# Performance work log

Measured on AMD Instinct MI355X. Metric: run time of the kernel, lower is better.

The kernel has to match this reference:

```python
import jax, jax.numpy as jnp
import numpy as np

R = 16
LORA_ALPHA = 16
SCALING = LORA_ALPHA / R  # 1.0


def setup_inputs() -> dict:
    key = jax.random.key(0)
    kx, kr, ka = jax.random.split(key, 3)
    B, S, D, DO, E = 4, 2048, 4096, 4096, 8
    x = jax.random.normal(kx, (B, S, D), dtype=jnp.float32)
    # kaiming_uniform_(a=sqrt(5)) on Linear weight of fan_in=D -> U(-1/sqrt(D), 1/sqrt(D))
    bound_r = 1.0 / np.sqrt(D)
    route_w = jax.random.uniform(kr, (E, D), jnp.float32, -bound_r, bound_r)  # lora_route.weight
    bound_a = 1.0 / np.sqrt(D)
    A = jax.random.uniform(ka, (E, R, D), jnp.float32, -bound_a, bound_a)  # stacked lora_A{i}.weight [r, D]
    # lora_B weights are zero-initialized in the module; use small random for a nontrivial baseline
    kb = jax.random.fold_in(key, 7)
    Bw = jax.random.normal(kb, (E, DO, R), dtype=jnp.float32) * 0.02  # stacked lora_B{i}.weight [DO, r]
    return {"x": x, "route_w": route_w, "A": A, "Bw": Bw}


def reference(x, route_w, A, Bw):
    # router logits [B, S, E]
    logits = jnp.einsum("bsd,ed->bse", x, route_w)
    # top-1 hard routing: keep raw logit value at the argmax slot, zero elsewhere
    topk_v, topk_idx = jax.lax.top_k(logits, 1)  # [B,S,1]
    E = logits.shape[-1]
    route_weight = jax.nn.one_hot(topk_idx[..., 0], E, dtype=logits.dtype) * topk_v  # [B,S,E]
    # low-rank per-expert projections (dense over experts, as in the original loop)
    h = jnp.einsum("bsd,erd->bser", x, A)            # [B,S,E,r]
    wh = route_weight[..., None] * h                  # weight before the up-projection
    out = jnp.einsum("bser,eor->bso", wh, Bw) * SCALING  # [B,S,DO]
    return out
```

## Files before the change

### kernel.cpp

```cpp
#include <hip/hip_runtime.h>
#include <hip/hip_bf16.h>

#define DD   4096
#define NE   8
#define NR   16
#define NTOK 8192
#define NDO  4096
#define TAU  0.01f
#define MAXFLAG 8000

typedef __attribute__((ext_vector_type(8))) __bf16 bf16x8;
typedef __attribute__((ext_vector_type(4))) float  f32x4;

__device__ __forceinline__ bf16x8 to_bf16x8(float4 a, float4 b) {
    bf16x8 r;
    r[0] = (__bf16)a.x; r[1] = (__bf16)a.y; r[2] = (__bf16)a.z; r[3] = (__bf16)a.w;
    r[4] = (__bf16)b.x; r[5] = (__bf16)b.y; r[6] = (__bf16)b.z; r[7] = (__bf16)b.w;
    return r;
}

__device__ __forceinline__ bf16x8 lo_bf16x8(float4 a, float4 b, bf16x8 h) {
    bf16x8 r;
    r[0] = (__bf16)(a.x - (float)h[0]); r[1] = (__bf16)(a.y - (float)h[1]);
    r[2] = (__bf16)(a.z - (float)h[2]); r[3] = (__bf16)(a.w - (float)h[3]);
    r[4] = (__bf16)(b.x - (float)h[4]); r[5] = (__bf16)(b.y - (float)h[5]);
    r[6] = (__bf16)(b.z - (float)h[6]); r[7] = (__bf16)(b.w - (float)h[7]);
    return r;
}

__device__ __forceinline__ bf16x8 zero_frag() {
    bf16x8 z;
    #pragma unroll
    for (int j = 0; j < 8; j++) z[j] = (__bf16)0.0f;
    return z;
}

__global__ __launch_bounds__(256) void k_prep(const float* __restrict__ x,
                                              const float* __restrict__ rw,
                                              const float* __restrict__ Am,
                                              const float* __restrict__ Bw,
                                              __bf16* __restrict__ xb,
                                              __bf16* __restrict__ rwhl,
                                              __bf16* __restrict__ Ab,
                                              __bf16* __restrict__ Bwb) {
    const int b = blockIdx.x;
    const float* src;  __bf16* dst;  size_t base;
    if (b < 4096)      { base = (size_t)b * 8192 + threadIdx.x * 32;            src = x;  dst = xb;  }
    else if (b < 4160) { base = (size_t)(b - 4096) * 8192 + threadIdx.x * 32;   src = Am; dst = Ab;  }
    else if (b < 4224) { base = (size_t)(b - 4160) * 8192 + threadIdx.x * 32;   src = Bw; dst = Bwb; }
    else {
        const int obase = (b - 4224) * 8192 + threadIdx.x * 32;
        const int row = obase >> 12, k = obase & 4095;
        const float* s = rw + ((size_t)(row & 7) << 12) + k;
        float4 v[8];
        #pragma unroll
        for (int i = 0; i < 8; i++) v[i] = *(const float4*)(s + i * 4);
        if (row < 8) {
            #pragma unroll
            for (int i = 0; i < 4; i++)
                *(bf16x8*)(rwhl + obase + i * 8) = to_bf16x8(v[2*i], v[2*i+1]);
        } else {
            #pragma unroll
            for (int i = 0; i < 4; i++) {
                const bf16x8 h = to_bf16x8(v[2*i], v[2*i+1]);
                *(bf16x8*)(rwhl + obase + i * 8) = lo_bf16x8(v[2*i], v[2*i+1], h);
            }
        }
        return;
    }
    float4 v[8];
    #pragma unroll
    for (int i = 0; i < 8; i++) v[i] = *(const float4*)(src + base + i * 4);
    #pragma unroll
    for (int i = 0; i < 4; i++)
        *(bf16x8*)(dst + base + i * 8) = to_bf16x8(v[2*i], v[2*i+1]);
}

__global__ __launch_bounds__(1024) void k_route(const __bf16* __restrict__ xb,
                                                const __bf16* __restrict__ rwhl,
                                                float* __restrict__ w_arr,
                                                int*   __restrict__ token_list,
                                                int*   __restrict__ count,
                                                int*   __restrict__ nflag,
                                                int*   __restrict__ flaglist) {
    const int t0   = blockIdx.x * 16;
    const int wv   = threadIdx.x >> 6;
    const int lane = threadIdx.x & 63;
    const int m    = lane & 15;
    const int half = lane >> 4;

    const __bf16* xrow = xb   + (size_t)(t0 + m) * DD;
    const __bf16* wrow = rwhl + (size_t)m * DD;

    f32x4 acc = {0.f, 0.f, 0.f, 0.f};
    const int kbase = wv * 256;
    #pragma unroll
    for (int ks = 0; ks < 8; ks++) {
        const int k0 = kbase + ks * 32 + half * 8;
        const bf16x8 a = *(const bf16x8*)(xrow + k0);
        const bf16x8 b = *(const bf16x8*)(wrow + k0);
        acc = __builtin_amdgcn_mfma_f32_16x16x32_bf16(a, b, acc, 0, 0, 0);
    }

    __shared__ float Lred[16][16][17];
    #pragma unroll
    for (int r = 0; r < 4; r++)
        Lred[wv][half * 4 + r][m] = acc[r];
    __syncthreads();

    __shared__ float logitS[16][NE];
    if (threadIdx.x < 128) {
        const int t = threadIdx.x >> 3, ee = threadIdx.x & 7;
        float s = 0.f;
        #pragma unroll
        for (int w = 0; w < 16; w++) s += Lred[w][t][ee] + Lred[w][t][ee + 8];
        logitS[t][ee] = s;
    }
    __syncthreads();

    if (threadIdx.x < 16) {
        const int t = threadIdx.x;
        float best = -1e30f, second = -1e30f; int be = 0;
        #pragma unroll
        for (int e = 0; e < NE; e++) {
            const float s = logitS[t][e];
            if (s > best) { second = best; best = s; be = e; }
            else if (s > second) { second = s; }
        }
        const int tok = t0 + t;
        w_arr[tok] = best;
        if (best - second < TAU) {
            const int p = atomicAdd(nflag, 1);
            if (p < MAXFLAG) flaglist[p] = tok;
        } else {
            const int p = atomicAdd(&count[be], 1);
            token_list[be * NTOK + p] = tok;
        }
    }
}

__global__ __launch_bounds__(256) void k_fix(const float* __restrict__ x,
                                             const float* __restrict__ rw,
                                             float* __restrict__ w_arr,
                                             int*   __restrict__ token_list,
                                             int*   __restrict__ count,
                                             const int* __restrict__ nflag,
                                             const int* __restrict__ flaglist) {
    const int wv   = threadIdx.x >> 6;
    const int lane = threadIdx.x & 63;
    int n = *nflag; if (n > MAXFLAG) n = MAXFLAG;

    for (int idx = blockIdx.x * 4 + wv; idx < n; idx += 512) {
        const int tok = flaglist[idx];
        const float* xp = x + (size_t)tok * DD;
        double acc[NE];
        #pragma unroll
        for (int e = 0; e < NE; e++) acc[e] = 0.0;
        for (int i = 0; i < 16; i++) {
            const int d4 = (i * 64 + lane) * 4;
            const float4 xv = *(const float4*)(xp + d4);
            const double x0 = xv.x, x1 = xv.y, x2 = xv.z, x3 = xv.w;
            #pragma unroll
            for (int e = 0; e < NE; e++) {
                const float4 wv4 = *(const float4*)(rw + (size_t)e * DD + d4);
                acc[e] = fma(x0, (double)wv4.x, acc[e]);
                acc[e] = fma(x1, (double)wv4.y, acc[e]);
                acc[e] = fma(x2, (double)wv4.z, acc[e]);
                acc[e] = fma(x3, (double)wv4.w, acc[e]);
            }
        }
        #pragma unroll
        for (int off = 32; off > 0; off >>= 1)
            #pragma unroll
            for (int e = 0; e < NE; e++)
                acc[e] += __shfl_xor(acc[e], off, 64);
        if (lane == 0) {
            double best = acc[0]; int be = 0;
            #pragma unroll
            for (int e = 1; e < NE; e++) if (acc[e] > best) { best = acc[e]; be = e; }
            w_arr[tok] = (float)best;
            const int pos = atomicAdd(&count[be], 1);
            token_list[be * NTOK + pos] = tok;
        }
    }
}

__global__ __launch_bounds__(1024) void k_h(const __bf16* __restrict__ xb,
                                            const __bf16* __restrict__ Ab,
                                            const float* __restrict__ w_arr,
                                            const int*   __restrict__ token_list,
                                            const int*   __restrict__ count,
                                            __hip_bfloat16* __restrict__ wh) {
    const int e    = blockIdx.x >> 7;
    const int g    = blockIdx.x & 127;
    const int cnt  = count[e];
    const int base = g * 32;
    if (base >= cnt) return;

    const int wv   = threadIdx.x >> 6;
    const int lane = threadIdx.x & 63;
    const int m    = lane & 15;
    const int half = lane >> 4;

    const int i0 = base + m,  i1 = base + 16 + m;
    const int tok0 = (i0 < cnt) ? token_list[e * NTOK + i0] : 0;
    const int tok1 = (i1 < cnt) ? token_list[e * NTOK + i1] : 0;
    const __bf16* xr0  = xb + (size_t)tok0 * DD;
    const __bf16* xr1  = xb + (size_t)tok1 * DD;
    const __bf16* arow = Ab + ((size_t)e * NR + m) * DD;

    f32x4 acc0 = {0.f,0.f,0.f,0.f}, acc1 = {0.f,0.f,0.f,0.f};
    const int kbase = wv * 256;
    #pragma unroll
    for (int kc = 0; kc < 8; kc++) {
        const int k0 = kbase + kc * 32 + half * 8;
        const bf16x8 bfrag = *(const bf16x8*)(arow + k0);
        const bf16x8 a0    = *(const bf16x8*)(xr0 + k0);
        const bf16x8 a1    = *(const bf16x8*)(xr1 + k0);
        acc0 = __builtin_amdgcn_mfma_f32_16x16x32_bf16(a0, bfrag, acc0, 0, 0, 0);
        acc1 = __builtin_amdgcn_mfma_f32_16x16x32_bf16(a1, bfrag, acc1, 0, 0, 0);
    }

    __shared__ float lds[16][32][17];
    #pragma unroll
    for (int rr = 0; rr < 4; rr++) {
        lds[wv][half * 4 + rr][m]      = acc0[rr];
        lds[wv][16 + half * 4 + rr][m] = acc1[rr];
    }
    __syncthreads();

    if (threadIdx.x < 512) {
        const int t = threadIdx.x >> 4;
        const int r = threadIdx.x & 15;
        const int i2 = base + t;
        if (i2 < cnt) {
            float s = 0.f;
            #pragma unroll
            for (int w = 0; w < 16; w++) s += lds[w][t][r];
            const int tk = token_list[e * NTOK + i2];
            wh[(size_t)tk * NR + r] = (__hip_bfloat16)(s * w_arr[tk]);
        }
    }
}

__global__ __launch_bounds__(256) void k_out(const __bf16* __restrict__ Bwb,
                                             const __hip_bfloat16* __restrict__ wh,
                                             const int*   __restrict__ token_list,
                                             const int*   __restrict__ count,
                                             float* __restrict__ out) {
    const int bx    = blockIdx.x;
    const int chunk = bx & 3;
    const int slot  = (bx >> 2) & 511;
    const int e     = bx >> 11;
    const int cnt   = count[e];
    const int base  = slot * 16;
    if (base >= cnt) return;

    const int wv   = threadIdx.x >> 6;
    const int lane = threadIdx.x & 63;
    const int m    = lane & 15;
    const int half = lane >> 4;

    const int  idx   = base + m;
    const bool valid = idx < cnt;
    const int  tok   = valid ? token_list[e * NTOK + idx] : 0;
    const bf16x8 zf  = zero_frag();

    bf16x8 a2 = (half < 2 && valid)
        ? *(const bf16x8*)((const __bf16*)wh + (size_t)tok * NR + half * 8)
        : zf;

    int trow[4]; bool vrow[4];
    #pragma unroll
    for (int r = 0; r < 4; r++) {
        const int ir = base + half * 4 + r;
        vrow[r] = ir < cnt;
        trow[r] = vrow[r] ? token_list[e * NTOK + ir] : 0;
    }

    const __bf16* bwe = Bwb + (size_t)e * NDO * NR;
    const int h2 = (half < 2) ? half : 0;
    const f32x4 zero4 = {0.f, 0.f, 0.f, 0.f};
    const int ob0 = chunk * 1024 + wv * 256;

    #pragma unroll 4
    for (int ot = 0; ot < 16; ot++) {
        const int obase = ob0 + ot * 16;
        const bf16x8 b2 = (half < 2)
            ? *(const bf16x8*)(bwe + (size_t)(obase + m) * NR + h2 * 8)
            : zf;
        const f32x4 d = __builtin_amdgcn_mfma_f32_16x16x32_bf16(a2, b2, zero4, 0, 0, 0);
        #pragma unroll
        for (int r = 0; r < 4; r++) {
            if (vrow[r]) out[(size_t)trow[r] * NDO + obase + m] = d[r];
        }
    }
}

extern "C" void kernel_launch(void* const* d_in, const int* in_sizes, int n_in,
                              void* d_out, int out_size, void* d_ws, size_t ws_size,
                              hipStream_t stream) {
    const float* x  = (const float*)d_in[0];
    const float* rw = (const float*)d_in[1];
    const float* Am = (const float*)d_in[2];
    const float* Bw = (const float*)d_in[3];
    float* out = (float*)d_out;

    char* ws = (char*)d_ws;
    int*   count      = (int*)ws;
    int*   nflag      = (int*)(ws + 32);
    float* w_arr      = (float*)(ws + 512);
    int*   flaglist   = (int*)(ws + 33280);
    int*   token_list = (int*)(ws + 65536);
    __hip_bfloat16* wh = (__hip_bfloat16*)(ws + 327680);
    __bf16* rwhl      = (__bf16*)(ws + 589824);
    __bf16* Bwb       = (__bf16*)(ws + 720896);
    __bf16* Ab        = (__bf16*)(ws + 1769472);
    __bf16* xb        = (__bf16*)(ws + 4194304);

    hipMemsetAsync(ws, 0, 64, stream);
    hipLaunchKernelGGL(k_prep,  dim3(4232),  dim3(256),  0, stream, x, rw, Am, Bw, xb, rwhl, Ab, Bwb);
    hipLaunchKernelGGL(k_route, dim3(512),   dim3(1024), 0, stream, xb, rwhl, w_arr, token_list, count, nflag, flaglist);
    hipLaunchKernelGGL(k_fix,   dim3(128),   dim3(256),  0, stream, x, rw, w_arr, token_list, count, nflag, flaglist);
    hipLaunchKernelGGL(k_h,     dim3(1024),  dim3(1024), 0, stream, xb, Ab, w_arr, token_list, count, wh);
    hipLaunchKernelGGL(k_out,   dim3(16384), dim3(256),  0, stream, Bwb, wh, token_list, count, out);
}
```

Before: 172.0 us.

## Drop bf16 copy of x and convert activations on the fly in route and h kernels

```diff
diff --git a/kernel.cpp b/kernel.cpp
--- a/kernel.cpp
+++ b/kernel.cpp
@@ -10,6 +10,7 @@
 #define MAXFLAG 8000
 
 typedef __attribute__((ext_vector_type(8))) __bf16 bf16x8;
+typedef __attribute__((ext_vector_type(4))) __bf16 bf16x4;
 typedef __attribute__((ext_vector_type(4))) float  f32x4;
 
 __device__ __forceinline__ bf16x8 to_bf16x8(float4 a, float4 b) {
@@ -19,15 +20,6 @@
     return r;
 }
 
-__device__ __forceinline__ bf16x8 lo_bf16x8(float4 a, float4 b, bf16x8 h) {
-    bf16x8 r;
-    r[0] = (__bf16)(a.x - (float)h[0]); r[1] = (__bf16)(a.y - (float)h[1]);
-    r[2] = (__bf16)(a.z - (float)h[2]); r[3] = (__bf16)(a.w - (float)h[3]);
-    r[4] = (__bf16)(b.x - (float)h[4]); r[5] = (__bf16)(b.y - (float)h[5]);
-    r[6] = (__bf16)(b.z - (float)h[6]); r[7] = (__bf16)(b.w - (float)h[7]);
-    return r;
-}
-
 __device__ __forceinline__ bf16x8 zero_frag() {
     bf16x8 z;
     #pragma unroll
@@ -35,74 +27,69 @@
     return z;
 }
 
-__global__ __launch_bounds__(256) void k_prep(const float* __restrict__ x,
-                                              const float* __restrict__ rw,
-                                              const float* __restrict__ Am,
-                                              const float* __restrict__ Bw,
-                                              __bf16* __restrict__ xb,
-                                              __bf16* __restrict__ rwhl,
-                                              __bf16* __restrict__ Ab,
-                                              __bf16* __restrict__ Bwb) {
+__global__ __launch_bounds__(256) void k_prep_w(const float* __restrict__ rw,
+                                                const float* __restrict__ Am,
+                                                const float* __restrict__ Bw,
+                                                __bf16* __restrict__ rwhl,
+                                                __bf16* __restrict__ Ab,
+                                                __bf16* __restrict__ Bwb) {
     const int b = blockIdx.x;
-    const float* src;  __bf16* dst;  size_t base;
-    if (b < 4096)      { base = (size_t)b * 8192 + threadIdx.x * 32;            src = x;  dst = xb;  }
-    else if (b < 4160) { base = (size_t)(b - 4096) * 8192 + threadIdx.x * 32;   src = Am; dst = Ab;  }
-    else if (b < 4224) { base = (size_t)(b - 4160) * 8192 + threadIdx.x * 32;   src = Bw; dst = Bwb; }
-    else {
-        const int obase = (b - 4224) * 8192 + threadIdx.x * 32;
-        const int row = obase >> 12, k = obase & 4095;
-        const float* s = rw + ((size_t)(row & 7) << 12) + k;
-        float4 v[8];
-        #pragma unroll
-        for (int i = 0; i < 8; i++) v[i] = *(const float4*)(s + i * 4);
+    if (b < 1024) {
+        const int o = (b & 511) * 1024 + threadIdx.x * 4;
+        const float4 v = *(const float4*)(((b < 512) ? Bw : Am) + o);
+        bf16x4 p;
+        p[0] = (__bf16)v.x; p[1] = (__bf16)v.y; p[2] = (__bf16)v.z; p[3] = (__bf16)v.w;
+        *(bf16x4*)(((b < 512) ? Bwb : Ab) + o) = p;
+    } else {
+        const int o = (b - 1024) * 1024 + threadIdx.x * 4;
+        const int row = o >> 12, k = o & 4095;
+        const float4 v = *(const float4*)(rw + ((size_t)(row & 7) << 12) + k);
+        bf16x4 p;
         if (row < 8) {
-            #pragma unroll
-            for (int i = 0; i < 4; i++)
-                *(bf16x8*)(rwhl + obase + i * 8) = to_bf16x8(v[2*i], v[2*i+1]);
+            p[0] = (__bf16)v.x; p[1] = (__bf16)v.y; p[2] = (__bf16)v.z; p[3] = (__bf16)v.w;
         } else {
-            #pragma unroll
-            for (int i = 0; i < 4; i++) {
-                const bf16x8 h = to_bf16x8(v[2*i], v[2*i+1]);
-                *(bf16x8*)(rwhl + obase + i * 8) = lo_bf16x8(v[2*i], v[2*i+1], h);
-            }
-        }
-        return;
-    }
-    float4 v[8];
-    #pragma unroll
-    for (int i = 0; i < 8; i++) v[i] = *(const float4*)(src + base + i * 4);
-    #pragma unroll
-    for (int i = 0; i < 4; i++)
-        *(bf16x8*)(dst + base + i * 8) = to_bf16x8(v[2*i], v[2*i+1]);
-}
-
-__global__ __launch_bounds__(1024) void k_route(const __bf16* __restrict__ xb,
-                                                const __bf16* __restrict__ rwhl,
-                                                float* __restrict__ w_arr,
-                                                int*   __restrict__ token_list,
-                                                int*   __restrict__ count,
-                                                int*   __restrict__ nflag,
-                                                int*   __restrict__ flaglist) {
+            p[0] = (__bf16)(v.x - (float)(__bf16)v.x);
+            p[1] = (__bf16)(v.y - (float)(__bf16)v.y);
+            p[2] = (__bf16)(v.z - (float)(__bf16)v.z);
+            p[3] = (__bf16)(v.w - (float)(__bf16)v.w);
+        }
+        *(bf16x4*)(rwhl + o) = p;
+    }
+}
+
+__global__ __launch_bounds__(256, 1) void k_route(const float* __restrict__ x,
+                                                  const __bf16* __restrict__ rwhl,
+                                                  float* __restrict__ w_arr,
+                                                  int*   __restrict__ token_list,
+                                                  int*   __restrict__ count,
+                                                  int*   __restrict__ nflag,
+                                                  int*   __restrict__ flaglist) {
     const int t0   = blockIdx.x * 16;
     const int wv   = threadIdx.x >> 6;
     const int lane = threadIdx.x & 63;
     const int m    = lane & 15;
     const int half = lane >> 4;
 
-    const __bf16* xrow = xb   + (size_t)(t0 + m) * DD;
+    const float*  xrow = x    + (size_t)(t0 + m) * DD;
     const __bf16* wrow = rwhl + (size_t)m * DD;
 
     f32x4 acc = {0.f, 0.f, 0.f, 0.f};
-    const int kbase = wv * 256;
-    #pragma unroll
-    for (int ks = 0; ks < 8; ks++) {
-        const int k0 = kbase + ks * 32 + half * 8;
-        const bf16x8 a = *(const bf16x8*)(xrow + k0);
-        const bf16x8 b = *(const bf16x8*)(wrow + k0);
-        acc = __builtin_amdgcn_mfma_f32_16x16x32_bf16(a, b, acc, 0, 0, 0);
-    }
-
-    __shared__ float Lred[16][16][17];
+    const int kbase = wv * 1024;
+    for (int g = 0; g < 8; g++) {
+        float4 xa[4], xc[4]; bf16x8 wb[4];
+        #pragma unroll
+        for (int i = 0; i < 4; i++) {
+            const int k0 = kbase + (g * 4 + i) * 32 + half * 8;
+            xa[i] = *(const float4*)(xrow + k0);
+            xc[i] = *(const float4*)(xrow + k0 + 4);
+            wb[i] = *(const bf16x8*)(wrow + k0);
+        }
+        #pragma unroll
+        for (int i = 0; i < 4; i++)
+            acc = __builtin_amdgcn_mfma_f32_16x16x32_bf16(to_bf16x8(xa[i], xc[i]), wb[i], acc, 0, 0, 0);
+    }
+
+    __shared__ float Lred[4][16][17];
     #pragma unroll
     for (int r = 0; r < 4; r++)
         Lred[wv][half * 4 + r][m] = acc[r];
@@ -113,7 +100,7 @@
         const int t = threadIdx.x >> 3, ee = threadIdx.x & 7;
         float s = 0.f;
         #pragma unroll
-        for (int w = 0; w < 16; w++) s += Lred[w][t][ee] + Lred[w][t][ee + 8];
+        for (int w = 0; w < 4; w++) s += Lred[w][t][ee] + Lred[w][t][ee + 8];
         logitS[t][ee] = s;
     }
     __syncthreads();
@@ -185,7 +172,7 @@
     }
 }
 
-__global__ __launch_bounds__(1024) void k_h(const __bf16* __restrict__ xb,
+__global__ __launch_bounds__(1024) void k_h(const float* __restrict__ x,
                                             const __bf16* __restrict__ Ab,
                                             const float* __restrict__ w_arr,
                                             const int*   __restrict__ token_list,
@@ -205,8 +192,8 @@
     const int i0 = base + m,  i1 = base + 16 + m;
     const int tok0 = (i0 < cnt) ? token_list[e * NTOK + i0] : 0;
     const int tok1 = (i1 < cnt) ? token_list[e * NTOK + i1] : 0;
-    const __bf16* xr0  = xb + (size_t)tok0 * DD;
-    const __bf16* xr1  = xb + (size_t)tok1 * DD;
+    const float*  xr0  = x  + (size_t)tok0 * DD;
+    const float*  xr1  = x  + (size_t)tok1 * DD;
     const __bf16* arow = Ab + ((size_t)e * NR + m) * DD;
 
     f32x4 acc0 = {0.f,0.f,0.f,0.f}, acc1 = {0.f,0.f,0.f,0.f};
@@ -215,8 +202,10 @@
     for (int kc = 0; kc < 8; kc++) {
         const int k0 = kbase + kc * 32 + half * 8;
         const bf16x8 bfrag = *(const bf16x8*)(arow + k0);
-        const bf16x8 a0    = *(const bf16x8*)(xr0 + k0);
-        const bf16x8 a1    = *(const bf16x8*)(xr1 + k0);
+        const bf16x8 a0 = to_bf16x8(*(const float4*)(xr0 + k0),
+                                    *(const float4*)(xr0 + k0 + 4));
+        const bf16x8 a1 = to_bf16x8(*(const float4*)(xr1 + k0),
+                                    *(const float4*)(xr1 + k0 + 4));
         acc0 = __builtin_amdgcn_mfma_f32_16x16x32_bf16(a0, bfrag, acc0, 0, 0, 0);
         acc1 = __builtin_amdgcn_mfma_f32_16x16x32_bf16(a1, bfrag, acc1, 0, 0, 0);
     }
@@ -243,11 +232,11 @@
     }
 }
 
-__global__ __launch_bounds__(256) void k_out(const __bf16* __restrict__ Bwb,
-                                             const __hip_bfloat16* __restrict__ wh,
-                                             const int*   __restrict__ token_list,
-                                             const int*   __restrict__ count,
-                                             float* __restrict__ out) {
+__global__ __launch_bounds__(256, 1) void k_out(const __bf16* __restrict__ Bwb,
+                                                const __hip_bfloat16* __restrict__ wh,
+                                                const int*   __restrict__ token_list,
+                                                const int*   __restrict__ count,
+                                                float* __restrict__ out) {
     const int bx    = blockIdx.x;
     const int chunk = bx & 3;
     const int slot  = (bx >> 2) & 511;
@@ -266,7 +255,7 @@
     const int  tok   = valid ? token_list[e * NTOK + idx] : 0;
     const bf16x8 zf  = zero_frag();
 
-    bf16x8 a2 = (half < 2 && valid)
+    const bf16x8 a2 = (half < 2 && valid)
         ? *(const bf16x8*)((const __bf16*)wh + (size_t)tok * NR + half * 8)
         : zf;
 
@@ -283,16 +272,24 @@
     const f32x4 zero4 = {0.f, 0.f, 0.f, 0.f};
     const int ob0 = chunk * 1024 + wv * 256;
 
-    #pragma unroll 4
-    for (int ot = 0; ot < 16; ot++) {
-        const int obase = ob0 + ot * 16;
-        const bf16x8 b2 = (half < 2)
-            ? *(const bf16x8*)(bwe + (size_t)(obase + m) * NR + h2 * 8)
-            : zf;
-        const f32x4 d = __builtin_amdgcn_mfma_f32_16x16x32_bf16(a2, b2, zero4, 0, 0, 0);
-        #pragma unroll
-        for (int r = 0; r < 4; r++) {
-            if (vrow[r]) out[(size_t)trow[r] * NDO + obase + m] = d[r];
+    for (int g = 0; g < 2; g++) {
+        bf16x8 B[8];
+        #pragma unroll
+        for (int i = 0; i < 8; i++) {
+            const int obase = ob0 + (g * 8 + i) * 16;
+            B[i] = (half < 2)
+                ? *(const bf16x8*)(bwe + (size_t)(obase + m) * NR + h2 * 8)
+                : zf;
+        }
+        #pragma unroll
+        for (int i = 0; i < 8; i++) {
+            const int obase = ob0 + (g * 8 + i) * 16;
+            const f32x4 d = __builtin_amdgcn_mfma_f32_16x16x32_bf16(a2, B[i], zero4, 0, 0, 0);
+            #pragma unroll
+            for (int r = 0; r < 4; r++) {
+                if (vrow[r])
+                    __builtin_nontemporal_store(d[r], &out[(size_t)trow[r] * NDO + obase + m]);
+            }
         }
     }
 }
@@ -316,12 +313,11 @@
     __bf16* rwhl      = (__bf16*)(ws + 589824);
     __bf16* Bwb       = (__bf16*)(ws + 720896);
     __bf16* Ab        = (__bf16*)(ws + 1769472);
-    __bf16* xb        = (__bf16*)(ws + 4194304);
 
     hipMemsetAsync(ws, 0, 64, stream);
-    hipLaunchKernelGGL(k_prep,  dim3(4232),  dim3(256),  0, stream, x, rw, Am, Bw, xb, rwhl, Ab, Bwb);
-    hipLaunchKernelGGL(k_route, dim3(512),   dim3(1024), 0, stream, xb, rwhl, w_arr, token_list, count, nflag, flaglist);
-    hipLaunchKernelGGL(k_fix,   dim3(128),   dim3(256),  0, stream, x, rw, w_arr, token_list, count, nflag, flaglist);
-    hipLaunchKernelGGL(k_h,     dim3(1024),  dim3(1024), 0, stream, xb, Ab, w_arr, token_list, count, wh);
-    hipLaunchKernelGGL(k_out,   dim3(16384), dim3(256),  0, stream, Bwb, wh, token_list, count, out);
-}
+    hipLaunchKernelGGL(k_prep_w, dim3(1088),  dim3(256),  0, stream, rw, Am, Bw, rwhl, Ab, Bwb);
+    hipLaunchKernelGGL(k_route,  dim3(512),   dim3(256),  0, stream, x, rwhl, w_arr, token_list, count, nflag, flaglist);
+    hipLaunchKernelGGL(k_fix,    dim3(128),   dim3(256),  0, stream, x, rw, w_arr, token_list, count, nflag, flaglist);
+    hipLaunchKernelGGL(k_h,      dim3(1024),  dim3(1024), 0, stream, x, Ab, w_arr, token_list, count, wh);
+    hipLaunchKernelGGL(k_out,    dim3(16384), dim3(256),  0, stream, Bwb, wh, token_list, count, out);
+}
```

After: 161.1 us. 6.3% less time.
